# Kernel tuning notes

Measured on AMD Instinct MI355X. Metric: run time of the kernel, lower is better.

## Reference

```python
import jax, jax.numpy as jnp
import numpy as np

B, T, D_IN, D_SAE, K = 256, 8, 768, 8192, 32


def setup_inputs() -> dict:
    key = jax.random.key(0)
    k1, k2, k3 = jax.random.split(key, 3)
    x = jax.random.normal(k1, (B, T, D_IN), dtype=jnp.float32)
    # kaiming_uniform: bound = sqrt(6 / fan_in), fan_in = prod of trailing dims
    bound_e = float(np.sqrt(6.0 / (D_SAE * D_IN)))
    W_enc = jax.random.uniform(k2, (T, D_SAE, D_IN), jnp.float32, -bound_e, bound_e)
    bound_d = float(np.sqrt(6.0 / (D_IN * D_SAE)))
    W_dec = jax.random.uniform(k3, (T, D_IN, D_SAE), jnp.float32, -bound_d, bound_d)
    # decoder column normalization (norm over d_in axis), as in _normalize_decoder
    norms = jnp.clip(jnp.linalg.norm(W_dec, axis=1, keepdims=True), 1e-8)
    W_dec = W_dec / norms
    b_enc = jnp.zeros((T, D_SAE), jnp.float32)
    b_dec = jnp.zeros((T, D_IN), jnp.float32)
    return {"x": x, "W_enc": W_enc, "b_enc": b_enc, "W_dec": W_dec,
            "b_dec": b_dec, "k": K}


def reference(x, W_enc, b_enc, W_dec, b_dec, k):
    # x: (B, T, d_in)
    x_c = x - b_dec[None]                                   # (B, T, d)
    pre = jnp.einsum('btd,thd->bth', x_c, W_enc) + b_enc[None]  # (B, T, h)
    bt = pre.shape[0] * pre.shape[1]
    pre_flat = pre.reshape(bt, -1)
    topk_vals, topk_idx = jax.lax.top_k(pre_flat, k)        # (BT, k)
    rows = jnp.arange(bt)[:, None]
    u_flat = jnp.zeros_like(pre_flat).at[rows, topk_idx].set(jax.nn.relu(topk_vals))
    u = u_flat.reshape(pre.shape)                            # (B, T, h)
    x_hat = jnp.einsum('bth,tdh->btd', u, W_dec) + b_dec[None]
    recon_loss = jnp.mean(jnp.sum((x_hat - x) ** 2, axis=-1))
    return recon_loss, x_hat, u
```

## Files before the change

kernel.cpp:

```cpp
#include <hip/hip_runtime.h>
#include <cstdint>
#include <cstddef>

constexpr int B_SZ  = 256;
constexpr int T_SZ  = 8;
constexpr int DIN   = 768;
constexpr int DSAE  = 8192;
constexpr int KSEL  = 32;
constexpr int NROWS = B_SZ * T_SZ;
constexpr int CAND_CAP = 64;
constexpr int RCAP  = 32;
constexpr float EPS_W = 5.5e-4f;
constexpr int NSK   = DIN / 32;

constexpr size_t XC_SZ    = (size_t)NROWS * DIN;
constexpr size_t OFF_XC   = 0;
constexpr size_t OFF_XCP  = OFF_XC + XC_SZ;
constexpr size_t XCP_W    = XC_SZ / 2;
constexpr size_t OFF_SIDX = OFF_XCP + XCP_W;
constexpr size_t OFF_SVAL = OFF_SIDX + (size_t)NROWS * KSEL;
constexpr size_t OFF_PREB = OFF_SVAL + (size_t)NROWS * KSEL;
constexpr size_t PREB_W   = (size_t)NROWS * DSAE / 2;
constexpr size_t OFF_BIG  = OFF_PREB + PREB_W;
constexpr size_t BIG_W    = (size_t)T_SZ * DSAE * DIN / 2;
constexpr size_t WS_FAST_WORDS = OFF_BIG + BIG_W;

typedef short bf16x8 __attribute__((ext_vector_type(8)));
typedef float f32x4  __attribute__((ext_vector_type(4)));

__device__ inline unsigned rne1(float x) {
  unsigned u = __float_as_uint(x);
  return (u + 0x7FFFu + ((u >> 16) & 1u)) >> 16;
}
__device__ inline float bf16tof(unsigned short v) {
  return __uint_as_float((unsigned)v << 16);
}
__device__ inline unsigned packtr(float a, float b) {
  return (__float_as_uint(a) >> 16) | (__float_as_uint(b) & 0xFFFF0000u);
}
__device__ inline void gload_lds16(const void* g, void* l) {
  __builtin_amdgcn_global_load_lds(
      (const __attribute__((address_space(1))) void*)g,
      (__attribute__((address_space(3))) void*)l, 16, 0, 0);
}

__global__ void k_zero(float* p) { *p = 0.f; }

__global__ __launch_bounds__(256) void k_uzero(float* __restrict__ u) {
  const size_t base = (size_t)(blockIdx.x * 256 + threadIdx.x) * 4;
  const size_t stride = (size_t)gridDim.x * 256 * 4;
  const float4 z = {0.f, 0.f, 0.f, 0.f};
  for (size_t i = base; i < (size_t)NROWS * DSAE; i += stride)
    *(float4*)(u + i) = z;
}

__global__ __launch_bounds__(256) void k_xc(const float* __restrict__ x,
                                            const float* __restrict__ bdec,
                                            float* __restrict__ xc,
                                            unsigned short* __restrict__ xcp) {
  const int c = blockIdx.x * 256 + threadIdx.x;
  const int lane = c & 63;
  const int u = c >> 6;
  const int s  = u % NSK;
  const int tt = (u / NSK) & (T_SZ - 1);
  const int gm = u / (NSK * T_SZ);
  const int b  = gm * 16 + (lane & 15);
  const int k0 = s * 32 + (lane >> 4) * 8;
  const size_t rowOff = ((size_t)(b * T_SZ + tt)) * DIN + k0;
  float4 v0 = *(const float4*)(x + rowOff);
  float4 v1 = *(const float4*)(x + rowOff + 4);
  float4 d0 = *(const float4*)(bdec + tt * DIN + k0);
  float4 d1 = *(const float4*)(bdec + tt * DIN + k0 + 4);
  v0.x -= d0.x; v0.y -= d0.y; v0.z -= d0.z; v0.w -= d0.w;
  v1.x -= d1.x; v1.y -= d1.y; v1.z -= d1.z; v1.w -= d1.w;
  *(float4*)(xc + rowOff) = v0;
  *(float4*)(xc + rowOff + 4) = v1;
  uint4 p;
  p.x = rne1(v0.x) | (rne1(v0.y) << 16);
  p.y = rne1(v0.z) | (rne1(v0.w) << 16);
  p.z = rne1(v1.x) | (rne1(v1.y) << 16);
  p.w = rne1(v1.z) | (rne1(v1.w) << 16);
  *(uint4*)(xcp + (size_t)c * 8) = p;
}

__global__ __launch_bounds__(256, 2) void k_encoder(const unsigned short* __restrict__ xcp,
                                                    const float* __restrict__ Wenc,
                                                    const float* __restrict__ benc,
                                                    unsigned short* __restrict__ preb) {
  __shared__ __align__(16) float Bs[4][64 * 32];
  const int tid = threadIdx.x;
  const int wm = tid >> 6, lane = tid & 63;
  const int l15 = lane & 15, kc = lane >> 4;

  int gRow[2], gCol[2], ldsL[2];
#pragma unroll
  for (int i = 0; i < 2; ++i) {
    int L = i * 4096 + tid * 16;
    int G = L ^ (((L >> 7) & 7) << 4);
    gRow[i] = G >> 7;
    gCol[i] = (G & 127) >> 2;
    ldsL[i] = L;
  }
  int bOff0[4], bOff1[4];
#pragma unroll
  for (int ni = 0; ni < 4; ++ni) {
    int row = ni * 16 + l15;
    int P = row * 128 + kc * 32;
    int sw = (row & 7) << 4;
    bOff0[ni] = P ^ sw;
    bOff1[ni] = (P + 16) ^ sw;
  }
  constexpr size_t A_MI = (size_t)T_SZ * NSK * 512;

  for (int tile = 0; tile < 2; ++tile) {
    const int tileId = blockIdx.x + tile * 512;
    const int t  = tileId >> 7;
    const int n0 = (tileId & 127) * 64;

    const float* bG = Wenc + ((size_t)t * DSAE + n0) * DIN;
    const unsigned short* aP =
        xcp + ((size_t)(wm * 4 * T_SZ + t) * NSK) * 512 + lane * 8;

    auto STAGE = [&](int buf, int s) {
#pragma unroll
      for (int i = 0; i < 2; ++i)
        gload_lds16(bG + (size_t)gRow[i] * DIN + s * 32 + gCol[i],
                    (char*)&Bs[0][0] + buf * 8192 + ldsL[i]);
    };

    f32x4 acc[4][4] = {};
    bf16x8 aA[4], aB[4];
    STAGE(0, 0);
#pragma unroll
    for (int mi = 0; mi < 4; ++mi)
      aA[mi] = *(const bf16x8*)(aP + mi * A_MI);
    STAGE(1, 1);

#define ENC_W6 asm volatile("s_waitcnt vmcnt(6)" ::: "memory")
#define ENC_W4 asm volatile("s_waitcnt vmcnt(4)" ::: "memory")
#define ENC_W0 asm volatile("s_waitcnt vmcnt(0)" ::: "memory")
#define ENC_STEP(u, PFB, PFA, WAITOP) do {                                   \
    if (PFB) STAGE(((u) + 2) & 3, s0 + (u) + 2);                             \
    if (PFA) {                                                               \
      const unsigned short* ap = aP + (size_t)(s0 + (u) + 1) * 512;          \
      _Pragma("unroll")                                                      \
      for (int mi = 0; mi < 4; ++mi) {                                       \
        bf16x8 v = *(const bf16x8*)(ap + mi * A_MI);                         \
        if ((u) % 2 == 0) aB[mi] = v; else aA[mi] = v;                       \
      }                                                                      \
    }                                                                        \
    __builtin_amdgcn_sched_barrier(0);                                       \
    WAITOP;                                                                  \
    __builtin_amdgcn_s_barrier();                                            \
    __builtin_amdgcn_sched_barrier(0);                                       \
    {                                                                        \
      const char* bb = (const char*)&Bs[0][0] + ((u) & 3) * 8192;            \
      _Pragma("unroll")                                                      \
      for (int ni = 0; ni < 4; ++ni) {                                       \
        f32x4 f0 = *(const f32x4*)(bb + bOff0[ni]);                          \
        f32x4 f1 = *(const f32x4*)(bb + bOff1[ni]);                          \
        union { uint32_t w[4]; bf16x8 h; } cvu;                              \
        cvu.w[0] = packtr(f0.x, f0.y); cvu.w[1] = packtr(f0.z, f0.w);        \
        cvu.w[2] = packtr(f1.x, f1.y); cvu.w[3] = packtr(f1.z, f1.w);        \
        _Pragma("unroll")                                                    \
        for (int mi = 0; mi < 4; ++mi)                                       \
          acc[mi][ni] = __builtin_amdgcn_mfma_f32_16x16x32_bf16(             \
              ((u) % 2 == 0) ? aA[mi] : aB[mi], cvu.h, acc[mi][ni], 0, 0, 0);\
      }                                                                      \
    }                                                                        \
  } while (0)

    int s0 = 0;
    for (int g = 0; g < 5; ++g, s0 += 4) {
      ENC_STEP(0, true, true, ENC_W6); ENC_STEP(1, true, true, ENC_W6);
      ENC_STEP(2, true, true, ENC_W6); ENC_STEP(3, true, true, ENC_W6);
    }
    ENC_STEP(0, true, true, ENC_W6);  ENC_STEP(1, true, true, ENC_W6);
    ENC_STEP(2, false, true, ENC_W4); ENC_STEP(3, false, false, ENC_W0);
#undef ENC_STEP
#undef ENC_W6
#undef ENC_W4
#undef ENC_W0

#pragma unroll
    for (int ni = 0; ni < 4; ++ni) {
      const int col = n0 + ni * 16 + l15;
      const float bias = benc[(size_t)t * DSAE + col];
#pragma unroll
      for (int mi = 0; mi < 4; ++mi) {
        const int rbase = wm * 64 + mi * 16 + kc * 4;
#pragma unroll
        for (int j = 0; j < 4; ++j)
          preb[((size_t)(rbase + j) * T_SZ + t) * DSAE + col] =
              (unsigned short)rne1(acc[mi][ni][j] + bias);
      }
    }
    if (tile == 0) __syncthreads();
  }
}

__global__ __launch_bounds__(256) void k_select(const float* __restrict__ xc,
                                                const float* __restrict__ Wenc,
                                                const float* __restrict__ benc,
                                                const unsigned short* __restrict__ preb,
                                                float* __restrict__ u,
                                                int* __restrict__ sel_idx,
                                                float* __restrict__ sel_val) {
  const int r = blockIdx.x, t = r & (T_SZ - 1);
  __shared__ float sp[DSAE];
  __shared__ float redf[4], redf2[4];
  __shared__ int   redi[4];
  __shared__ float cv[CAND_CAP]; __shared__ int ci[CAND_CAP];
  __shared__ float sv[CAND_CAP]; __shared__ int si[CAND_CAP];
  __shared__ float rv[RCAP];     __shared__ int ri[RCAP];
  __shared__ double rd[RCAP];
  __shared__ double xd[DIN];
  __shared__ int   s_n, s_nR, s_A, s_nW;
  const int tid = threadIdx.x, lane = tid & 63, w = tid >> 6;

  float s1 = 0.f, s2 = 0.f;
#pragma unroll
  for (int sgm = 0; sgm < 4; ++sgm) {
    const int i0 = sgm * 2048 + tid * 8;
    uint4 pk = *(const uint4*)(preb + (size_t)r * DSAE + i0);
    const unsigned wds[4] = {pk.x, pk.y, pk.z, pk.w};
#pragma unroll
    for (int q = 0; q < 4; ++q) {
      float lo = __uint_as_float(wds[q] << 16);
      float hi = __uint_as_float(wds[q] & 0xFFFF0000u);
      sp[i0 + q * 2 + 0] = lo;
      sp[i0 + q * 2 + 1] = hi;
      s1 += lo + hi; s2 = fmaf(lo, lo, fmaf(hi, hi, s2));
    }
  }
  for (int off = 32; off; off >>= 1) {
    s1 += __shfl_down(s1, off); s2 += __shfl_down(s2, off);
  }
  if (lane == 0) { redf[w] = s1; redf2[w] = s2; }
  __syncthreads();
  const float mean = (redf[0] + redf[1] + redf[2] + redf[3]) * (1.f / DSAE);
  const float var  = (redf2[0] + redf2[1] + redf2[2] + redf2[3]) * (1.f / DSAE) - mean * mean;
  const float sd   = sqrtf(fmaxf(var, 1e-20f));

  auto countGE = [&](float th) -> int {
    int c = 0;
#pragma unroll
    for (int sgm = 0; sgm < DSAE / 256; ++sgm)
      c += (sp[tid + sgm * 256] >= th) ? 1 : 0;
    for (int off = 32; off; off >>= 1) c += __shfl_down(c, off);
    __syncthreads();
    if (lane == 0) redi[w] = c;
    __syncthreads();
    return redi[0] + redi[1] + redi[2] + redi[3];
  };

  float tlo = mean + 2.0f * sd, thi = mean + 3.5f * sd;
  for (int it = 0; it < 8 && countGE(tlo) < KSEL; ++it) tlo -= sd;
  float th = mean + 2.52f * sd;
  int c = countGE(th);
  for (int it = 0; it < 24 && (c < KSEL || c > CAND_CAP); ++it) {
    if (c > CAND_CAP) tlo = th; else thi = th;
    th = 0.5f * (tlo + thi);
    c = countGE(th);
  }
  if (c < KSEL) { th = tlo; c = countGE(th); }

  if (tid == 0) s_n = 0;
  __syncthreads();
  for (int sgm = 0; sgm < DSAE / 256; ++sgm) {
    int i = tid + sgm * 256;
    float v = sp[i];
    if (v >= th) {
      int p = atomicAdd(&s_n, 1);
      if (p < CAND_CAP) { cv[p] = v; ci[p] = i; }
    }
  }
  __syncthreads();
  const int n = s_n < CAND_CAP ? s_n : CAND_CAP;

  if (tid < n) {
    float v = cv[tid]; int id = ci[tid];
    int rk = 0;
    for (int j = 0; j < n; ++j) {
      float vj = cv[j];
      rk += (vj > v || (vj == v && ci[j] < id)) ? 1 : 0;
    }
    sv[rk] = v; si[rk] = id;
  }
  __syncthreads();

  const float v32 = sv[KSEL - 1];
  const float wlo = v32 - EPS_W, whi = v32 + EPS_W;
  if (tid == 0) {
    int A = 0;
    while (A < KSEL - 1 && sv[A] > whi) ++A;
    s_A = A;
    int e = A;
    while (e < n && sv[e] >= wlo) ++e;
    s_nW = e - A;
  }
  __syncthreads();
  const int A  = s_A;
  const int nW = s_nW < RCAP ? s_nW : RCAP;
  if (tid < nW) { rv[tid] = sv[A + tid]; ri[tid] = si[A + tid]; }
  if (tid == 0) s_nR = nW;
  __syncthreads();
  if (th > wlo) {
    for (int sgm = 0; sgm < DSAE / 256; ++sgm) {
      int i = tid + sgm * 256;
      float v = sp[i];
      if (v >= wlo && v < th) {
        int p = atomicAdd(&s_nR, 1);
        if (p < RCAP) { rv[p] = v; ri[p] = i; }
      }
    }
  }
  __syncthreads();
  const int nR = s_nR < RCAP ? s_nR : RCAP;

  if (nR >= 2) {
    for (int i = tid; i < DIN; i += 256) xd[i] = (double)xc[(size_t)r * DIN + i];
    __syncthreads();
    for (int j = w; j < nR; j += 4) {
      const int h = ri[j];
      const float* wrow = Wenc + ((size_t)t * DSAE + h) * DIN;
      double s = 0.0;
#pragma unroll
      for (int ss = 0; ss < DIN / 64; ++ss)
        s += xd[lane + 64 * ss] * (double)wrow[lane + 64 * ss];
      for (int off = 32; off; off >>= 1) s += __shfl_down(s, off);
      if (lane == 0) rd[j] = s + (double)benc[(size_t)t * DSAE + h];
    }
  } else if (nR == 1) {
    if (tid == 0) rd[0] = (double)rv[0];
  }
  __syncthreads();

  float* urow = u + (size_t)r * DSAE;
  if (tid < A) {
    float val = fmaxf(sv[tid], 0.f);
    urow[si[tid]] = val;
    sel_idx[(size_t)r * KSEL + tid] = si[tid];
    sel_val[(size_t)r * KSEL + tid] = val;
  }
  const int need = KSEL - A;
  if (tid < nR) {
    double v = rd[tid]; int id = ri[tid];
    int rk = 0;
    for (int j = 0; j < nR; ++j) {
      double vj = rd[j];
      rk += (vj > v || (vj == v && ri[j] < id)) ? 1 : 0;
    }
    if (rk < need) {
      float val = fmaxf((float)v, 0.f);
      urow[id] = val;
      sel_idx[(size_t)r * KSEL + A + rk] = id;
      sel_val[(size_t)r * KSEL + A + rk] = val;
    }
  }
}

__global__ __launch_bounds__(256) void k_transpose(const float* __restrict__ W,
                                                   unsigned short* __restrict__ Wt) {
  __shared__ unsigned short tile[128 * 137];
  const int h0 = blockIdx.x * 128;
  const int d0 = blockIdx.y * 128;
  const int t  = blockIdx.z;
  const int tid = threadIdx.x;
  const float* src = W + ((size_t)t * DIN + d0) * DSAE + h0;
#pragma unroll
  for (int i = 0; i < 16; ++i) {
    const int F = (i * 256 + tid) * 4;
    const int r = F >> 7, c = F & 127;
    float4 v = *(const float4*)(src + (size_t)r * DSAE + c);
    unsigned short* p = &tile[r * 137 + c];
    p[0] = (unsigned short)rne1(v.x); p[1] = (unsigned short)rne1(v.y);
    p[2] = (unsigned short)rne1(v.z); p[3] = (unsigned short)rne1(v.w);
  }
  __syncthreads();
#pragma unroll
  for (int j = 0; j < 16; ++j) {
    const int E  = j * 256 + tid;
    const int hr = E >> 5;
    const int dc = (E & 31) * 4;
    unsigned a = (unsigned)tile[(dc + 0) * 137 + hr] |
                 ((unsigned)tile[(dc + 1) * 137 + hr] << 16);
    unsigned b = (unsigned)tile[(dc + 2) * 137 + hr] |
                 ((unsigned)tile[(dc + 3) * 137 + hr] << 16);
    uint2 o; o.x = a; o.y = b;
    *(uint2*)(Wt + ((size_t)(t * DSAE + h0 + hr)) * DIN + d0 + dc) = o;
  }
}

template <bool TRANSPOSED>
__global__ __launch_bounds__(256) void k_decoder(const void* __restrict__ Wd_,
                                                 const float* __restrict__ x,
                                                 const float* __restrict__ bdec,
                                                 const int* __restrict__ sel_idx,
                                                 const float* __restrict__ sel_val,
                                                 float* __restrict__ xhat,
                                                 float* __restrict__ loss) {
  const int r = blockIdx.x, t = r & (T_SZ - 1);
  __shared__ int   si[KSEL];
  __shared__ float sv[KSEL];
  __shared__ float rbuf[4];
  const int tid = threadIdx.x;
  if (tid < KSEL) {
    si[tid] = sel_idx[(size_t)r * KSEL + tid] & (DSAE - 1);
    sv[tid] = sel_val[(size_t)r * KSEL + tid];
  }
  __syncthreads();

  float acc[3];
#pragma unroll
  for (int i = 0; i < 3; ++i) acc[i] = bdec[(size_t)t * DIN + tid + 256 * i];
#pragma unroll 4
  for (int j = 0; j < KSEL; ++j) {
    const int h = si[j];
    const float v = sv[j];
    if (TRANSPOSED) {
      const unsigned short* wrow =
          (const unsigned short*)Wd_ + ((size_t)t * DSAE + h) * DIN;
#pragma unroll
      for (int i = 0; i < 3; ++i)
        acc[i] = fmaf(v, bf16tof(wrow[tid + 256 * i]), acc[i]);
    } else {
      const float* Wd = (const float*)Wd_;
#pragma unroll
      for (int i = 0; i < 3; ++i)
        acc[i] = fmaf(v, Wd[((size_t)t * DIN + tid + 256 * i) * DSAE + h], acc[i]);
    }
  }
  float sq = 0.f;
#pragma unroll
  for (int i = 0; i < 3; ++i) {
    const int d = tid + 256 * i;
    const float xv = x[(size_t)r * DIN + d];
    xhat[(size_t)r * DIN + d] = acc[i];
    const float e = acc[i] - xv;
    sq = fmaf(e, e, sq);
  }
  for (int off = 32; off; off >>= 1) sq += __shfl_down(sq, off);
  if ((tid & 63) == 0) rbuf[tid >> 6] = sq;
  __syncthreads();
  if (tid == 0)
    atomicAdd(loss, (rbuf[0] + rbuf[1] + rbuf[2] + rbuf[3]) * (1.0f / NROWS));
}

extern "C" void kernel_launch(void* const* d_in, const int* in_sizes, int n_in,
                              void* d_out, int out_size, void* d_ws, size_t ws_size,
                              hipStream_t stream) {
  const float* x    = (const float*)d_in[0];
  const float* Wenc = (const float*)d_in[1];
  const float* benc = (const float*)d_in[2];
  const float* Wdec = (const float*)d_in[3];
  const float* bdec = (const float*)d_in[4];

  float* out  = (float*)d_out;
  float* loss = out;
  float* xhat = out + 1;
  float* u    = out + 1 + (size_t)NROWS * DIN;

  float*          wsf  = (float*)d_ws;
  float*          xc   = wsf + OFF_XC;
  unsigned short* xcp  = (unsigned short*)(wsf + OFF_XCP);
  int*            sidx = (int*)(wsf + OFF_SIDX);
  float*          sval = wsf + OFF_SVAL;
  unsigned short* preb = (unsigned short*)(wsf + OFF_PREB);
  unsigned short* big  = (unsigned short*)(wsf + OFF_BIG);
  const bool fast = ws_size >= WS_FAST_WORDS * sizeof(float);

  k_zero<<<1, 1, 0, stream>>>(loss);
  k_uzero<<<2048, 256, 0, stream>>>(u);
  k_xc<<<NROWS * DIN / (256 * 8), 256, 0, stream>>>(x, bdec, xc, xcp);
  k_encoder<<<512, 256, 0, stream>>>(xcp, Wenc, benc, preb);
  k_select<<<NROWS, 256, 0, stream>>>(xc, Wenc, benc, preb, u, sidx, sval);
  if (fast) {
    k_transpose<<<dim3(DSAE / 128, DIN / 128, T_SZ), 256, 0, stream>>>(Wdec, big);
    k_decoder<true><<<NROWS, 256, 0, stream>>>(big, x, bdec, sidx, sval, xhat, loss);
  } else {
    k_decoder<false><<<NROWS, 256, 0, stream>>>(Wdec, x, bdec, sidx, sval, xhat, loss);
  }
}
```

Before: 234.0 us.

## Fuse init kernels, co-schedule decoder transpose with encoder, fuse select+decode

```diff
diff --git a/kernel.cpp b/kernel.cpp
--- a/kernel.cpp
+++ b/kernel.cpp
@@ -17,9 +17,7 @@
 constexpr size_t OFF_XC   = 0;
 constexpr size_t OFF_XCP  = OFF_XC + XC_SZ;
 constexpr size_t XCP_W    = XC_SZ / 2;
-constexpr size_t OFF_SIDX = OFF_XCP + XCP_W;
-constexpr size_t OFF_SVAL = OFF_SIDX + (size_t)NROWS * KSEL;
-constexpr size_t OFF_PREB = OFF_SVAL + (size_t)NROWS * KSEL;
+constexpr size_t OFF_PREB = OFF_XCP + XCP_W;
 constexpr size_t PREB_W   = (size_t)NROWS * DSAE / 2;
 constexpr size_t OFF_BIG  = OFF_PREB + PREB_W;
 constexpr size_t BIG_W    = (size_t)T_SZ * DSAE * DIN / 2;
@@ -44,26 +42,28 @@
       (__attribute__((address_space(3))) void*)l, 16, 0, 0);
 }
 
-__global__ void k_zero(float* p) { *p = 0.f; }
-
-__global__ __launch_bounds__(256) void k_uzero(float* __restrict__ u) {
-  const size_t base = (size_t)(blockIdx.x * 256 + threadIdx.x) * 4;
-  const size_t stride = (size_t)gridDim.x * 256 * 4;
-  const float4 z = {0.f, 0.f, 0.f, 0.f};
-  for (size_t i = base; i < (size_t)NROWS * DSAE; i += stride)
-    *(float4*)(u + i) = z;
-}
-
-__global__ __launch_bounds__(256) void k_xc(const float* __restrict__ x,
-                                            const float* __restrict__ bdec,
-                                            float* __restrict__ xc,
-                                            unsigned short* __restrict__ xcp) {
-  const int c = blockIdx.x * 256 + threadIdx.x;
+__global__ __launch_bounds__(256) void k_init(const float* __restrict__ x,
+                                              const float* __restrict__ bdec,
+                                              float* __restrict__ xc,
+                                              unsigned short* __restrict__ xcp,
+                                              float* __restrict__ u,
+                                              float* __restrict__ loss) {
+  const int tid = threadIdx.x;
+  if (blockIdx.x < 2048) {
+    if (blockIdx.x == 0 && tid == 0) *loss = 0.f;
+    const size_t base = (size_t)(blockIdx.x * 256 + tid) * 4;
+    const size_t stride = (size_t)2048 * 256 * 4;
+    const float4 z = {0.f, 0.f, 0.f, 0.f};
+    for (size_t i = base; i < (size_t)NROWS * DSAE; i += stride)
+      *(float4*)(u + i) = z;
+    return;
+  }
+  const int c = (blockIdx.x - 2048) * 256 + tid;
   const int lane = c & 63;
-  const int u = c >> 6;
-  const int s  = u % NSK;
-  const int tt = (u / NSK) & (T_SZ - 1);
-  const int gm = u / (NSK * T_SZ);
+  const int uu = c >> 6;
+  const int s  = uu % NSK;
+  const int tt = (uu / NSK) & (T_SZ - 1);
+  const int gm = uu / (NSK * T_SZ);
   const int b  = gm * 16 + (lane & 15);
   const int k0 = s * 32 + (lane >> 4) * 8;
   const size_t rowOff = ((size_t)(b * T_SZ + tt)) * DIN + k0;
@@ -83,12 +83,50 @@
   *(uint4*)(xcp + (size_t)c * 8) = p;
 }
 
-__global__ __launch_bounds__(256, 2) void k_encoder(const unsigned short* __restrict__ xcp,
-                                                    const float* __restrict__ Wenc,
-                                                    const float* __restrict__ benc,
-                                                    unsigned short* __restrict__ preb) {
-  __shared__ __align__(16) float Bs[4][64 * 32];
+__global__ __launch_bounds__(256, 4) void k_enc_trans(
+    const unsigned short* __restrict__ xcp,
+    const float* __restrict__ Wenc,
+    const float* __restrict__ benc,
+    unsigned short* __restrict__ preb,
+    const float* __restrict__ Wdec,
+    unsigned short* __restrict__ wt) {
+  __shared__ __align__(16) char smem[35072];
   const int tid = threadIdx.x;
+
+  if (blockIdx.x >= 512) {
+    unsigned short* tile = (unsigned short*)smem;
+    const int tb = blockIdx.x - 512;
+    const int h0 = (tb & 63) * 128;
+    const int rem = tb >> 6;
+    const int d0 = (rem % 6) * 128;
+    const int t  = rem / 6;
+    const float* src = Wdec + ((size_t)t * DIN + d0) * DSAE + h0;
+#pragma unroll
+    for (int i = 0; i < 16; ++i) {
+      const int F = (i * 256 + tid) * 4;
+      const int r = F >> 7, c = F & 127;
+      float4 v = *(const float4*)(src + (size_t)r * DSAE + c);
+      unsigned short* p = &tile[r * 137 + c];
+      p[0] = (unsigned short)rne1(v.x); p[1] = (unsigned short)rne1(v.y);
+      p[2] = (unsigned short)rne1(v.z); p[3] = (unsigned short)rne1(v.w);
+    }
+    __syncthreads();
+#pragma unroll
+    for (int j = 0; j < 16; ++j) {
+      const int E  = j * 256 + tid;
+      const int hr = E >> 5;
+      const int dc = (E & 31) * 4;
+      unsigned a = (unsigned)tile[(dc + 0) * 137 + hr] |
+                   ((unsigned)tile[(dc + 1) * 137 + hr] << 16);
+      unsigned b = (unsigned)tile[(dc + 2) * 137 + hr] |
+                   ((unsigned)tile[(dc + 3) * 137 + hr] << 16);
+      uint2 o; o.x = a; o.y = b;
+      *(uint2*)(wt + ((size_t)(t * DSAE + h0 + hr)) * DIN + d0 + dc) = o;
+    }
+    return;
+  }
+
+  float* Bs = (float*)smem;
   const int wm = tid >> 6, lane = tid & 63;
   const int l15 = lane & 15, kc = lane >> 4;
 
@@ -125,7 +163,7 @@
 #pragma unroll
       for (int i = 0; i < 2; ++i)
         gload_lds16(bG + (size_t)gRow[i] * DIN + s * 32 + gCol[i],
-                    (char*)&Bs[0][0] + buf * 8192 + ldsL[i]);
+                    (char*)Bs + buf * 8192 + ldsL[i]);
     };
 
     f32x4 acc[4][4] = {};
@@ -154,7 +192,7 @@
     __builtin_amdgcn_s_barrier();                                            \
     __builtin_amdgcn_sched_barrier(0);                                       \
     {                                                                        \
-      const char* bb = (const char*)&Bs[0][0] + ((u) & 3) * 8192;            \
+      const char* bb = (const char*)Bs + ((u) & 3) * 8192;                   \
       _Pragma("unroll")                                                      \
       for (int ni = 0; ni < 4; ++ni) {                                       \
         f32x4 f0 = *(const f32x4*)(bb + bOff0[ni]);                          \
@@ -199,13 +237,18 @@
   }
 }
 
-__global__ __launch_bounds__(256) void k_select(const float* __restrict__ xc,
-                                                const float* __restrict__ Wenc,
-                                                const float* __restrict__ benc,
-                                                const unsigned short* __restrict__ preb,
-                                                float* __restrict__ u,
-                                                int* __restrict__ sel_idx,
-                                                float* __restrict__ sel_val) {
+template <bool TRANSPOSED>
+__global__ __launch_bounds__(256) void k_select_dec(
+    const float* __restrict__ xc,
+    const float* __restrict__ Wenc,
+    const float* __restrict__ benc,
+    const unsigned short* __restrict__ preb,
+    const void* __restrict__ Wd_,
+    const float* __restrict__ x,
+    const float* __restrict__ bdec,
+    float* __restrict__ u,
+    float* __restrict__ xhat,
+    float* __restrict__ loss) {
   const int r = blockIdx.x, t = r & (T_SZ - 1);
   __shared__ float sp[DSAE];
   __shared__ float redf[4], redf2[4];
@@ -215,6 +258,9 @@
   __shared__ float rv[RCAP];     __shared__ int ri[RCAP];
   __shared__ double rd[RCAP];
   __shared__ double xd[DIN];
+  __shared__ int   dsi[KSEL];
+  __shared__ float dsv[KSEL];
+  __shared__ float rbuf[4];
   __shared__ int   s_n, s_nR, s_A, s_nW;
   const int tid = threadIdx.x, lane = tid & 63, w = tid >> 6;
 
@@ -340,8 +386,7 @@
   if (tid < A) {
     float val = fmaxf(sv[tid], 0.f);
     urow[si[tid]] = val;
-    sel_idx[(size_t)r * KSEL + tid] = si[tid];
-    sel_val[(size_t)r * KSEL + tid] = val;
+    dsi[tid] = si[tid]; dsv[tid] = val;
   }
   const int need = KSEL - A;
   if (tid < nR) {
@@ -354,60 +399,8 @@
     if (rk < need) {
       float val = fmaxf((float)v, 0.f);
       urow[id] = val;
-      sel_idx[(size_t)r * KSEL + A + rk] = id;
-      sel_val[(size_t)r * KSEL + A + rk] = val;
-    }
-  }
-}
-
-__global__ __launch_bounds__(256) void k_transpose(const float* __restrict__ W,
-                                                   unsigned short* __restrict__ Wt) {
-  __shared__ unsigned short tile[128 * 137];
-  const int h0 = blockIdx.x * 128;
-  const int d0 = blockIdx.y * 128;
-  const int t  = blockIdx.z;
-  const int tid = threadIdx.x;
-  const float* src = W + ((size_t)t * DIN + d0) * DSAE + h0;
-#pragma unroll
-  for (int i = 0; i < 16; ++i) {
-    const int F = (i * 256 + tid) * 4;
-    const int r = F >> 7, c = F & 127;
-    float4 v = *(const float4*)(src + (size_t)r * DSAE + c);
-    unsigned short* p = &tile[r * 137 + c];
-    p[0] = (unsigned short)rne1(v.x); p[1] = (unsigned short)rne1(v.y);
-    p[2] = (unsigned short)rne1(v.z); p[3] = (unsigned short)rne1(v.w);
-  }
-  __syncthreads();
-#pragma unroll
-  for (int j = 0; j < 16; ++j) {
-    const int E  = j * 256 + tid;
-    const int hr = E >> 5;
-    const int dc = (E & 31) * 4;
-    unsigned a = (unsigned)tile[(dc + 0) * 137 + hr] |
-                 ((unsigned)tile[(dc + 1) * 137 + hr] << 16);
-    unsigned b = (unsigned)tile[(dc + 2) * 137 + hr] |
-                 ((unsigned)tile[(dc + 3) * 137 + hr] << 16);
-    uint2 o; o.x = a; o.y = b;
-    *(uint2*)(Wt + ((size_t)(t * DSAE + h0 + hr)) * DIN + d0 + dc) = o;
-  }
-}
-
-template <bool TRANSPOSED>
-__global__ __launch_bounds__(256) void k_decoder(const void* __restrict__ Wd_,
-                                                 const float* __restrict__ x,
-                                                 const float* __restrict__ bdec,
-                                                 const int* __restrict__ sel_idx,
-                                                 const float* __restrict__ sel_val,
-                                                 float* __restrict__ xhat,
-                                                 float* __restrict__ loss) {
-  const int r = blockIdx.x, t = r & (T_SZ - 1);
-  __shared__ int   si[KSEL];
-  __shared__ float sv[KSEL];
-  __shared__ float rbuf[4];
-  const int tid = threadIdx.x;
-  if (tid < KSEL) {
-    si[tid] = sel_idx[(size_t)r * KSEL + tid] & (DSAE - 1);
-    sv[tid] = sel_val[(size_t)r * KSEL + tid];
+      dsi[A + rk] = id; dsv[A + rk] = val;
+    }
   }
   __syncthreads();
 
@@ -416,8 +409,8 @@
   for (int i = 0; i < 3; ++i) acc[i] = bdec[(size_t)t * DIN + tid + 256 * i];
 #pragma unroll 4
   for (int j = 0; j < KSEL; ++j) {
-    const int h = si[j];
-    const float v = sv[j];
+    const int h = dsi[j] & (DSAE - 1);
+    const float v = dsv[j];
     if (TRANSPOSED) {
       const unsigned short* wrow =
           (const unsigned short*)Wd_ + ((size_t)t * DSAE + h) * DIN;
@@ -464,21 +457,18 @@
   float*          wsf  = (float*)d_ws;
   float*          xc   = wsf + OFF_XC;
   unsigned short* xcp  = (unsigned short*)(wsf + OFF_XCP);
-  int*            sidx = (int*)(wsf + OFF_SIDX);
-  float*          sval = wsf + OFF_SVAL;
   unsigned short* preb = (unsigned short*)(wsf + OFF_PREB);
   unsigned short* big  = (unsigned short*)(wsf + OFF_BIG);
   const bool fast = ws_size >= WS_FAST_WORDS * sizeof(float);
 
-  k_zero<<<1, 1, 0, stream>>>(loss);
-  k_uzero<<<2048, 256, 0, stream>>>(u);
-  k_xc<<<NROWS * DIN / (256 * 8), 256, 0, stream>>>(x, bdec, xc, xcp);
-  k_encoder<<<512, 256, 0, stream>>>(xcp, Wenc, benc, preb);
-  k_select<<<NROWS, 256, 0, stream>>>(xc, Wenc, benc, preb, u, sidx, sval);
+  k_init<<<2816, 256, 0, stream>>>(x, bdec, xc, xcp, u, loss);
   if (fast) {
-    k_transpose<<<dim3(DSAE / 128, DIN / 128, T_SZ), 256, 0, stream>>>(Wdec, big);
-    k_decoder<true><<<NROWS, 256, 0, stream>>>(big, x, bdec, sidx, sval, xhat, loss);
+    k_enc_trans<<<512 + 3072, 256, 0, stream>>>(xcp, Wenc, benc, preb, Wdec, big);
+    k_select_dec<true><<<NROWS, 256, 0, stream>>>(xc, Wenc, benc, preb, big,
+                                                  x, bdec, u, xhat, loss);
   } else {
-    k_decoder<false><<<NROWS, 256, 0, stream>>>(Wdec, x, bdec, sidx, sval, xhat, loss);
-  }
-}
+    k_enc_trans<<<512, 256, 0, stream>>>(xcp, Wenc, benc, preb, Wdec, big);
+    k_select_dec<false><<<NROWS, 256, 0, stream>>>(xc, Wenc, benc, preb, Wdec,
+                                                   x, bdec, u, xhat, loss);
+  }
+}
```

New measurement: 338.4 us. +44.6%, slower.
